# Kernel optimization log

Hardware: AMD Instinct MI355X
Metric: run time of the kernel (lower is better)

## Reference

```python
import jax, jax.numpy as jnp
import numpy as np

D_MODEL = 256
NHEAD = 8
NUM_EXPERTS = 5
LQ, LK, BATCH = 100, 1024, 16
LN_EPS = 1e-5


def setup_inputs() -> dict:
    key = jax.random.key(0)
    ks = jax.random.split(key, 12)
    d, E = D_MODEL, NUM_EXPERTS
    s = 1.0 / np.sqrt(d)
    return {
        "tgt": jax.random.normal(ks[0], (LQ, BATCH, d), jnp.float32),
        "memory": jax.random.normal(ks[1], (LK, BATCH, d), jnp.float32),
        "query_pos": jax.random.normal(ks[2], (LQ, BATCH, d), jnp.float32),
        "pos": jax.random.normal(ks[3], (LK, BATCH, d), jnp.float32),
        # per-expert MultiheadAttention params (packed q,k,v in_proj like torch)
        "w_in": jax.random.normal(ks[4], (E, 3 * d, d), jnp.float32) * s,
        "b_in": jnp.zeros((E, 3 * d), jnp.float32),
        "w_out": jax.random.normal(ks[5], (E, d, d), jnp.float32) * s,
        "b_out": jnp.zeros((E, d), jnp.float32),
        # gating network
        "w_gate": jax.random.normal(ks[6], (E, d), jnp.float32) * s,
        "b_gate": jnp.zeros((E,), jnp.float32),
        # LayerNorm
        "ln_gamma": jnp.ones((d,), jnp.float32),
        "ln_beta": jnp.zeros((d,), jnp.float32),
    }


def _moe_cross_attn(tgt, memory, query_pos, pos, w_in, b_in, w_out, b_out,
                    w_gate, b_gate, ln_gamma, ln_beta):
    Lq, B, d = tgt.shape
    H = NHEAD
    hd = d // H
    E = w_in.shape[0]
    Lk = memory.shape[0]

    # gating over (seq*batch, d) -> softmax over experts
    gate = jax.nn.softmax(tgt @ w_gate.T + b_gate, axis=-1)  # (Lq, B, E)

    q_emb = tgt + query_pos      # (Lq, B, d)
    k_emb = memory + pos         # (Lk, B, d)

    wq, wk, wv = w_in[:, :d], w_in[:, d:2 * d], w_in[:, 2 * d:]
    bq, bk, bv = b_in[:, :d], b_in[:, d:2 * d], b_in[:, 2 * d:]

    # batched projections across all experts (replaces python loop of MHA calls)
    q = jnp.einsum('lbd,eod->elbo', q_emb, wq) + bq[:, None, None, :]
    k = jnp.einsum('sbd,eod->esbo', k_emb, wk) + bk[:, None, None, :]
    v = jnp.einsum('sbd,eod->esbo', memory, wv) + bv[:, None, None, :]

    q = q.reshape(E, Lq, B, H, hd) * (1.0 / np.sqrt(hd))
    k = k.reshape(E, Lk, B, H, hd)
    v = v.reshape(E, Lk, B, H, hd)

    scores = jnp.einsum('elbhk,esbhk->ebhls', q, k)      # (E, B, H, Lq, Lk)
    attn = jax.nn.softmax(scores, axis=-1)
    ctx = jnp.einsum('ebhls,esbhk->elbhk', attn, v).reshape(E, Lq, B, d)

    out = jnp.einsum('elbd,eod->elbo', ctx, w_out) + b_out[:, None, None, :]

    # softmax-gated weighted combine of expert outputs
    mo = jnp.einsum('lbe,elbd->lbd', gate, out)

    x = tgt + mo  # dropout is identity (p=0.0)
    mu = jnp.mean(x, axis=-1, keepdims=True)
    var = jnp.var(x, axis=-1, keepdims=True)
    return (x - mu) * jax.lax.rsqrt(var + LN_EPS) * ln_gamma + ln_beta


def reference(tgt, memory, query_pos, pos, w_in, b_in, w_out, b_out,
              w_gate, b_gate, ln_gamma, ln_beta):
    return _moe_cross_attn(tgt, memory, query_pos, pos, w_in, b_in, w_out,
                           b_out, w_gate, b_gate, ln_gamma, ln_beta)
```

## Files before the change

### kernel.cpp

```cpp
#include <hip/hip_runtime.h>


typedef __bf16 bf16x8 __attribute__((ext_vector_type(8)));
typedef float f32x4 __attribute__((ext_vector_type(4)));
typedef unsigned int u32x4 __attribute__((ext_vector_type(4)));
typedef unsigned int u32x2 __attribute__((ext_vector_type(2)));
typedef unsigned short u16x4 __attribute__((ext_vector_type(4)));
typedef unsigned short us;

__device__ __forceinline__ us f2bf(float f) {
    unsigned u = __builtin_bit_cast(unsigned, f);
    u += 0x7FFFu + ((u >> 16) & 1u);
    return (us)(u >> 16);
}

__device__ __forceinline__ unsigned pack2(float lo, float hi) {
    return (unsigned)f2bf(lo) | ((unsigned)f2bf(hi) << 16);
}

__device__ __forceinline__ float bf2f(us v) {
    unsigned u = ((unsigned)v) << 16;
    return __builtin_bit_cast(float, u);
}

__device__ __forceinline__ bf16x8 ld_bf8(const us* p) {
    return __builtin_bit_cast(bf16x8, *reinterpret_cast<const u32x4*>(p));
}

__device__ __forceinline__ void gld_lds16(const us* g, us* l) {
    __builtin_amdgcn_global_load_lds(
        (const __attribute__((address_space(1))) unsigned int*)g,
        (__attribute__((address_space(3))) unsigned int*)l, 16, 0, 0);
}

__launch_bounds__(256)
__global__ void cvt_all(const float* __restrict__ tgt, const float* __restrict__ qpos,
                        const float* __restrict__ mem, const float* __restrict__ pos,
                        const float* __restrict__ w_in, const float* __restrict__ w_out,
                        const float* __restrict__ w_gate, const float* __restrict__ b_gate,
                        us* __restrict__ Aq, us* __restrict__ Ak, us* __restrict__ Av,
                        us* __restrict__ Wb, us* __restrict__ WOb,
                        float* __restrict__ Gate)
{
    const int bid = blockIdx.x;
    const int tid = threadIdx.x;
    if (bid < 400) {
        const int i = bid * 256 + tid;
        const int lane = tid & 63;
        const int row = i >> 6;
        f32x4 a = reinterpret_cast<const f32x4*>(tgt)[i];
        f32x4 b = reinterpret_cast<const f32x4*>(qpos)[i];
        u16x4 r;
#pragma unroll
        for (int j = 0; j < 4; ++j) r[j] = f2bf(a[j] + b[j]);
        reinterpret_cast<u16x4*>(Aq)[i] = r;
        float g[5];
#pragma unroll
        for (int e = 0; e < 5; ++e) {
            f32x4 wg = *reinterpret_cast<const f32x4*>(w_gate + e * 256 + 4 * lane);
            float p = a[0] * wg[0] + a[1] * wg[1] + a[2] * wg[2] + a[3] * wg[3];
#pragma unroll
            for (int off = 32; off >= 1; off >>= 1) p += __shfl_xor(p, off, 64);
            g[e] = p + b_gate[e];
        }
        float mx = g[0];
#pragma unroll
        for (int e = 1; e < 5; ++e) mx = fmaxf(mx, g[e]);
        float sm = 0.0f;
#pragma unroll
        for (int e = 0; e < 5; ++e) { g[e] = __expf(g[e] - mx); sm += g[e]; }
        const float invs = 1.0f / sm;
        if (lane == 0) {
#pragma unroll
            for (int e = 0; e < 5; ++e) Gate[row * 5 + e] = g[e] * invs;
        }
    } else if (bid < 4496) {
        int i = (bid - 400) * 256 + tid;
        f32x4 m = reinterpret_cast<const f32x4*>(mem)[i];
        f32x4 p = reinterpret_cast<const f32x4*>(pos)[i];
        u16x4 rk, rv;
#pragma unroll
        for (int j = 0; j < 4; ++j) { rk[j] = f2bf(m[j] + p[j]); rv[j] = f2bf(m[j]); }
        reinterpret_cast<u16x4*>(Ak)[i] = rk;
        reinterpret_cast<u16x4*>(Av)[i] = rv;
    } else if (bid < 5456) {
        int i = (bid - 4496) * 256 + tid;
        f32x4 a = reinterpret_cast<const f32x4*>(w_in)[i];
        u16x4 r;
#pragma unroll
        for (int j = 0; j < 4; ++j) r[j] = f2bf(a[j]);
        reinterpret_cast<u16x4*>(Wb)[i] = r;
    } else {
        int i = (bid - 5456) * 256 + tid;
        f32x4 a = reinterpret_cast<const f32x4*>(w_out)[i];
        u16x4 r;
#pragma unroll
        for (int j = 0; j < 4; ++j) r[j] = f2bf(a[j]);
        reinterpret_cast<u16x4*>(WOb)[i] = r;
    }
}

template <bool BF16OUT>
__device__ __forceinline__ void gemm_body(const us* __restrict__ A,
                                          const us* __restrict__ W,
                                          const float* __restrict__ bias,
                                          void* __restrict__ Cout,
                                          float scale, int M)
{
    const int row0 = blockIdx.x * 128;
    const int col0 = blockIdx.y * 128;
    __shared__ us As[2 * 8192];
    __shared__ us Bs[2 * 8192];
    const int tid  = threadIdx.x;
    const int lane = tid & 63;
    const int w    = tid >> 6;
    const int l15  = lane & 15;
    const int quad = lane >> 4;
    const int wm   = (w >> 1) * 64;
    const int wn   = (w & 1) * 64;
    const int srow = lane >> 3;
    const int gofs = ((lane & 7) ^ srow) * 8;

    auto stage = [&](int buf, int kt) {
#pragma unroll
        for (int cc = 0; cc < 4; ++cc) {
            const int c = w * 4 + cc;
            const int row = c * 8 + srow;
            gld_lds16(A + (size_t)(row0 + row) * 256 + kt * 64 + gofs,
                      &As[buf * 8192 + c * 512]);
            gld_lds16(W + (size_t)(col0 + row) * 256 + kt * 64 + gofs,
                      &Bs[buf * 8192 + c * 512]);
        }
    };

    f32x4 acc[4][4] = {};

    auto compute = [&](int cur) {
#pragma unroll
        for (int kh = 0; kh < 2; ++kh) {
            bf16x8 af[4], bf[4];
#pragma unroll
            for (int mi = 0; mi < 4; ++mi) {
                const int row = wm + mi * 16 + l15;
                const int seg = (kh * 4 + quad) ^ (row & 7);
                af[mi] = ld_bf8(&As[cur * 8192 + row * 64 + seg * 8]);
            }
#pragma unroll
            for (int ni = 0; ni < 4; ++ni) {
                const int col = wn + ni * 16 + l15;
                const int seg = (kh * 4 + quad) ^ (col & 7);
                bf[ni] = ld_bf8(&Bs[cur * 8192 + col * 64 + seg * 8]);
            }
#pragma unroll
            for (int mi = 0; mi < 4; ++mi)
#pragma unroll
                for (int ni = 0; ni < 4; ++ni)
                    acc[mi][ni] = __builtin_amdgcn_mfma_f32_16x16x32_bf16(bf[ni], af[mi], acc[mi][ni], 0, 0, 0);
        }
    };

    stage(0, 0);
    stage(1, 1);

#pragma unroll
    for (int kt = 0; kt < 4; ++kt) {
        const int cur = kt & 1;
        if (kt < 3) asm volatile("s_waitcnt vmcnt(8)" ::: "memory");
        else        asm volatile("s_waitcnt vmcnt(0)" ::: "memory");
        __builtin_amdgcn_s_barrier();
        __builtin_amdgcn_sched_barrier(0);
        compute(cur);
        if (kt < 2) {
            asm volatile("s_waitcnt lgkmcnt(0)" ::: "memory");
            __builtin_amdgcn_sched_barrier(0);
            __builtin_amdgcn_s_barrier();
            __builtin_amdgcn_sched_barrier(0);
            stage(cur, kt + 2);
        }
    }

#pragma unroll
    for (int mi = 0; mi < 4; ++mi) {
        const int row = row0 + wm + mi * 16 + l15;
        if (row < M) {
#pragma unroll
            for (int ni = 0; ni < 4; ++ni) {
                const int colb = col0 + wn + ni * 16 + quad * 4;
                const f32x4 b4 = *reinterpret_cast<const f32x4*>(bias + colb);
                if constexpr (BF16OUT) {
                    u32x2 pk;
                    pk[0] = pack2((acc[mi][ni][0] + b4[0]) * scale,
                                  (acc[mi][ni][1] + b4[1]) * scale);
                    pk[1] = pack2((acc[mi][ni][2] + b4[2]) * scale,
                                  (acc[mi][ni][3] + b4[3]) * scale);
                    *reinterpret_cast<u32x2*>(reinterpret_cast<us*>(Cout) + (size_t)row * 256 + colb) = pk;
                } else {
                    f32x4 v;
#pragma unroll
                    for (int r = 0; r < 4; ++r) v[r] = (acc[mi][ni][r] + b4[r]) * scale;
                    *reinterpret_cast<f32x4*>(reinterpret_cast<float*>(Cout) + (size_t)row * 256 + colb) = v;
                }
            }
        }
    }
}

__launch_bounds__(256)
__global__ void gemm_qkv(const us* __restrict__ Aq, const us* __restrict__ Ak,
                         const us* __restrict__ Av, const us* __restrict__ Wb,
                         const float* __restrict__ b_in,
                         us* __restrict__ Qb, us* __restrict__ Kb, us* __restrict__ Vb)
{
    const int z = blockIdx.z;
    if (z < 5) {
        if (blockIdx.x >= 13) return;
        gemm_body<true>(Aq, Wb + (size_t)z * 196608, b_in + (size_t)z * 768,
                        Qb + (size_t)z * 409600, 0.17677669529663687f, 1600);
    } else if (z < 10) {
        const int e = z - 5;
        gemm_body<true>(Ak, Wb + 65536 + (size_t)e * 196608, b_in + (size_t)e * 768 + 256,
                        Kb + (size_t)e * 4194304, 1.0f, 16384);
    } else {
        const int e = z - 10;
        gemm_body<true>(Av, Wb + 131072 + (size_t)e * 196608, b_in + (size_t)e * 768 + 512,
                        Vb + (size_t)e * 4194304, 1.0f, 16384);
    }
}

__launch_bounds__(256)
__global__ void gemm_og(const us* __restrict__ PO, const float* __restrict__ PL,
                        const us* __restrict__ WOb, const float* __restrict__ b_out,
                        float* __restrict__ OUTf)
{
    const int e = blockIdx.z;
    const us* W = WOb + (size_t)e * 65536;
    const float* bias = b_out + (size_t)e * 256;
    float* Cout = OUTf + (size_t)e * 409600;

    const int row0 = blockIdx.x * 128;
    const int col0 = blockIdx.y * 128;
    __shared__ us As[2 * 8192];
    __shared__ us Bs[2 * 8192];
    const int tid  = threadIdx.x;
    const int lane = tid & 63;
    const int w    = tid >> 6;
    const int l15  = lane & 15;
    const int quad = lane >> 4;
    const int wm   = (w >> 1) * 64;
    const int wn   = (w & 1) * 64;
    const int srow = lane >> 3;
    const int gofs = ((lane & 7) ^ srow) * 8;

    u32x4 POr[4][4];
    float Lr[4];

    auto loadA = [&](int kt) {
#pragma unroll
        for (int cc = 0; cc < 4; ++cc) {
            const int c = w * 4 + cc;
            int grow = row0 + c * 8 + srow;
            if (grow > 1599) grow = 1599;
            const int d0 = kt * 64 + gofs;
            const size_t base = (size_t)e * 409600 + (size_t)grow * 256 + d0;
#pragma unroll
            for (int s = 0; s < 4; ++s)
                POr[cc][s] = *reinterpret_cast<const u32x4*>(PO + base + (size_t)s * 2048000);
            const int l = grow >> 4, bb = grow & 15, h = d0 >> 5;
            float L = 0.0f;
#pragma unroll
            for (int s = 0; s < 4; ++s)
                L += PL[((((size_t)s * 5 + e) * 16 + bb) * 8 + h) * 128 + l];
            Lr[cc] = L;
        }
    };
    auto writeA = [&](int buf) {
#pragma unroll
        for (int cc = 0; cc < 4; ++cc) {
            const float inv = 1.0f / Lr[cc];
            u32x4 pk;
#pragma unroll
            for (int j = 0; j < 4; ++j) {
                float v0 = 0.0f, v1 = 0.0f;
#pragma unroll
                for (int s = 0; s < 4; ++s) {
                    const unsigned u = POr[cc][s][j];
                    v0 += __builtin_bit_cast(float, u << 16);
                    v1 += __builtin_bit_cast(float, u & 0xffff0000u);
                }
                pk[j] = pack2(v0 * inv, v1 * inv);
            }
            *reinterpret_cast<u32x4*>(&As[buf * 8192 + (w * 4 + cc) * 512 + lane * 8]) = pk;
        }
    };
    auto loadW = [&](int buf, int kt) {
#pragma unroll
        for (int cc = 0; cc < 4; ++cc) {
            const int c = w * 4 + cc;
            const int row = c * 8 + srow;
            gld_lds16(W + (size_t)(col0 + row) * 256 + kt * 64 + gofs,
                      &Bs[buf * 8192 + c * 512]);
        }
    };

    loadA(0);
    loadW(0, 0);
    writeA(0);
    __syncthreads();

    f32x4 acc[4][4] = {};

#pragma unroll
    for (int kt = 0; kt < 4; ++kt) {
        const int cur = kt & 1;
        if (kt < 3) {
            loadA(kt + 1);
            loadW(cur ^ 1, kt + 1);
        }
#pragma unroll
        for (int kh = 0; kh < 2; ++kh) {
            bf16x8 af[4], bf[4];
#pragma unroll
            for (int mi = 0; mi < 4; ++mi) {
                const int row = wm + mi * 16 + l15;
                const int seg = (kh * 4 + quad) ^ (row & 7);
                af[mi] = ld_bf8(&As[cur * 8192 + row * 64 + seg * 8]);
            }
#pragma unroll
            for (int ni = 0; ni < 4; ++ni) {
                const int col = wn + ni * 16 + l15;
                const int seg = (kh * 4 + quad) ^ (col & 7);
                bf[ni] = ld_bf8(&Bs[cur * 8192 + col * 64 + seg * 8]);
            }
#pragma unroll
            for (int mi = 0; mi < 4; ++mi)
#pragma unroll
                for (int ni = 0; ni < 4; ++ni)
                    acc[mi][ni] = __builtin_amdgcn_mfma_f32_16x16x32_bf16(bf[ni], af[mi], acc[mi][ni], 0, 0, 0);
        }
        if (kt < 3) {
            writeA(cur ^ 1);
            __syncthreads();
        }
    }

#pragma unroll
    for (int mi = 0; mi < 4; ++mi) {
        const int row = row0 + wm + mi * 16 + l15;
        if (row < 1600) {
#pragma unroll
            for (int ni = 0; ni < 4; ++ni) {
                const int colb = col0 + wn + ni * 16 + quad * 4;
                const f32x4 b4 = *reinterpret_cast<const f32x4*>(bias + colb);
                f32x4 v;
#pragma unroll
                for (int r = 0; r < 4; ++r) v[r] = acc[mi][ni][r] + b4[r];
                *reinterpret_cast<f32x4*>(Cout + (size_t)row * 256 + colb) = v;
            }
        }
    }
}

__device__ __forceinline__ int vrow(int d) { return d * 264 + 8 * (d >> 3); }

__launch_bounds__(512)
__global__ void attn(const us* __restrict__ Qb, const us* __restrict__ Kb,
                     const us* __restrict__ Vb, us* __restrict__ PO,
                     float* __restrict__ PL)
{
    const int h = blockIdx.x;
    const int z = blockIdx.y;
    const int s = blockIdx.z;
    const int e = z >> 4, b = z & 15;
    const int tid  = threadIdx.x;
    const int w    = tid >> 6;
    const int lane = tid & 63;
    const int l15  = lane & 15, quad = lane >> 4;
    __shared__ us Ks[256 * 32];
    __shared__ us Vs[8464];
    __shared__ us Ps[7][16 * 40];

    const int key0 = s * 256;
    {
        const int kl  = lane >> 2;
        const int seg = lane & 3;
        const us* kg = Kb + ((size_t)((e * 1024 + key0 + w * 16 + kl) * 16 + b)) * 256
                          + h * 32 + seg * 8;
        gld_lds16(kg, &Ks[w * 512]);
        gld_lds16(kg + (size_t)128 * 16 * 256, &Ks[4096 + w * 512]);

        const int kv = tid >> 2;
        const int sg = tid & 3;
        const us* vg = Vb + ((size_t)((e * 1024 + key0 + kv) * 16 + b)) * 256
                          + h * 32 + sg * 8;
        u32x4 v0 = *reinterpret_cast<const u32x4*>(vg);
        u32x4 v1 = *reinterpret_cast<const u32x4*>(vg + (size_t)128 * 16 * 256);
#pragma unroll
        for (int j = 0; j < 4; ++j) {
            const int d0 = sg * 8 + 2 * j;
            const int e0 = vrow(d0);
            const int e1 = e0 + 264;
            Vs[e0 + kv]       = (us)(v0[j] & 0xffff);
            Vs[e1 + kv]       = (us)(v0[j] >> 16);
            Vs[e0 + 128 + kv] = (us)(v1[j] & 0xffff);
            Vs[e1 + 128 + kv] = (us)(v1[j] >> 16);
        }
    }
    u32x4 qraw = {0u, 0u, 0u, 0u};
    if (w < 7) {
        const int l = w * 16 + l15;
        if (l < 100)
            qraw = *reinterpret_cast<const u32x4*>(
                Qb + ((size_t)((e * 100 + l) * 16 + b)) * 256 + h * 32 + quad * 8);
    }
    const bf16x8 qf = __builtin_bit_cast(bf16x8, qraw);

    __syncthreads();

    if (w >= 7) return;

    const f32x4 zacc = {};
    f32x4 o0 = {}, o1 = {};
    float lsum = 0.0f;

    for (int c = 0; c < 8; ++c) {
        bf16x8 kf0 = ld_bf8(&Ks[(c * 32 + l15) * 32 + quad * 8]);
        bf16x8 kf1 = ld_bf8(&Ks[(c * 32 + 16 + l15) * 32 + quad * 8]);
        f32x4 s0 = __builtin_amdgcn_mfma_f32_16x16x32_bf16(kf0, qf, zacc, 0, 0, 0);
        f32x4 s1 = __builtin_amdgcn_mfma_f32_16x16x32_bf16(kf1, qf, zacc, 0, 0, 0);
        float p0[4], p1[4];
#pragma unroll
        for (int r = 0; r < 4; ++r) {
            p0[r] = __expf(s0[r]);
            p1[r] = __expf(s1[r]);
            lsum += p0[r] + p1[r];
        }
        u32x2 w0, w1;
        w0[0] = pack2(p0[0], p0[1]);
        w0[1] = pack2(p0[2], p0[3]);
        w1[0] = pack2(p1[0], p1[1]);
        w1[1] = pack2(p1[2], p1[3]);
        *reinterpret_cast<u32x2*>(&Ps[w][l15 * 40 + quad * 4])      = w0;
        *reinterpret_cast<u32x2*>(&Ps[w][l15 * 40 + 16 + quad * 4]) = w1;
        bf16x8 pf  = ld_bf8(&Ps[w][l15 * 40 + quad * 8]);
        bf16x8 vf0 = ld_bf8(&Vs[vrow(l15) + c * 32 + quad * 8]);
        bf16x8 vf1 = ld_bf8(&Vs[vrow(16 + l15) + c * 32 + quad * 8]);
        o0 = __builtin_amdgcn_mfma_f32_16x16x32_bf16(pf, vf0, o0, 0, 0, 0);
        o1 = __builtin_amdgcn_mfma_f32_16x16x32_bf16(pf, vf1, o1, 0, 0, 0);
    }

    lsum += __shfl_xor(lsum, 16, 64);
    lsum += __shfl_xor(lsum, 32, 64);

#pragma unroll
    for (int r = 0; r < 4; ++r) {
        const int row = w * 16 + quad * 4 + r;
        if (row < 100) {
            const size_t o = (((size_t)((s * 5 + e) * 100 + row)) * 16 + b) * 256 + h * 32;
            PO[o + l15]      = f2bf(o0[r]);
            PO[o + 16 + l15] = f2bf(o1[r]);
        }
    }
    const int q = w * 16 + l15;
    if (quad == 0 && q < 100)
        PL[((((size_t)s * 5 + e) * 16 + b) * 8 + h) * 128 + q] = lsum;
}

__launch_bounds__(256)
__global__ void finalize(const float* __restrict__ tgt, const float* __restrict__ Gate,
                         const float* __restrict__ OUTf,
                         const float* __restrict__ gamma, const float* __restrict__ beta,
                         float* __restrict__ out)
{
    const int row = blockIdx.x;
    const int d = threadIdx.x;
    __shared__ float red[8];
    const float t = tgt[(size_t)row * 256 + d];

    float mo = 0.0f;
#pragma unroll
    for (int e = 0; e < 5; ++e)
        mo += Gate[row * 5 + e] * OUTf[((size_t)e * 1600 + row) * 256 + d];
    const float x = t + mo;

    float p1 = x, p2 = x * x;
#pragma unroll
    for (int off = 32; off >= 1; off >>= 1) {
        p1 += __shfl_xor(p1, off, 64);
        p2 += __shfl_xor(p2, off, 64);
    }
    if ((d & 63) == 0) { red[d >> 6] = p1; red[4 + (d >> 6)] = p2; }
    __syncthreads();
    const float mean = (red[0] + red[1] + red[2] + red[3]) * (1.0f / 256.0f);
    const float msq  = (red[4] + red[5] + red[6] + red[7]) * (1.0f / 256.0f);
    const float var  = msq - mean * mean;

    out[(size_t)row * 256 + d] = (x - mean) * rsqrtf(var + 1e-5f) * gamma[d] + beta[d];
}

extern "C" void kernel_launch(void* const* d_in, const int* in_sizes, int n_in,
                              void* d_out, int out_size, void* d_ws, size_t ws_size,
                              hipStream_t stream)
{
    const float* tgt    = (const float*)d_in[0];
    const float* mem    = (const float*)d_in[1];
    const float* qpos   = (const float*)d_in[2];
    const float* pos    = (const float*)d_in[3];
    const float* w_in   = (const float*)d_in[4];
    const float* b_in   = (const float*)d_in[5];
    const float* w_out  = (const float*)d_in[6];
    const float* b_out  = (const float*)d_in[7];
    const float* w_gate = (const float*)d_in[8];
    const float* b_gate = (const float*)d_in[9];
    const float* ln_g   = (const float*)d_in[10];
    const float* ln_b   = (const float*)d_in[11];
    float* out = (float*)d_out;

    char* p = (char*)d_ws;
    auto alloc = [&](size_t n) { char* r = p; p += (n + 255) & ~(size_t)255; return r; };

    us* Aq   = (us*)alloc(409600ull * 2);
    us* Ak   = (us*)alloc(4194304ull * 2);
    us* Av   = (us*)alloc(4194304ull * 2);
    us* Wb   = (us*)alloc(983040ull * 2);
    us* WOb  = (us*)alloc(327680ull * 2);
    us* Qb   = (us*)alloc(5ull * 409600 * 2);
    us* Kb   = (us*)alloc(5ull * 4194304 * 2);
    us* Vb   = (us*)alloc(5ull * 4194304 * 2);
    float* OUTf  = (float*)alloc(5ull * 409600 * 4);
    float* Gate  = (float*)alloc(1600ull * 5 * 4);
    us*    PO = (us*)d_ws;
    float* PL = (float*)((char*)d_ws + 16384000);

    cvt_all<<<5776, 256, 0, stream>>>(tgt, qpos, mem, pos, w_in, w_out,
                                      w_gate, b_gate, Aq, Ak, Av, Wb, WOb, Gate);

    gemm_qkv<<<dim3(128, 2, 15), 256, 0, stream>>>(Aq, Ak, Av, Wb, b_in, Qb, Kb, Vb);

    attn<<<dim3(8, 80, 4), 512, 0, stream>>>(Qb, Kb, Vb, PO, PL);

    gemm_og<<<dim3(13, 2, 5), 256, 0, stream>>>(PO, PL, WOb, b_out, OUTf);

    finalize<<<1600, 256, 0, stream>>>(tgt, Gate, OUTf, ln_g, ln_b, out);
}
```

Baseline: 207.7 us.

## Restructure QKV GEMM to keep A tile resident and loop over experts

The QKV projection kernel now loads a full 128x256 activation tile into LDS once per block and loops over all five experts, streaming weight fragments straight from global memory into registers with a three-buffer rotation. This replaces the previous 3D grid, in which each expert and column half re-staged the same activation rows through LDS, and aims to cut redundant activation traffic and launch a much smaller grid. In exchange, each block does five times more work with a larger accumulator set (8x4 tiles), which raises register pressure. The grid drops to 269 blocks, which may underfill the GPU's compute units and leaves the weight loads exposed to global memory latency.

```diff
diff --git a/kernel.cpp b/kernel.cpp
--- a/kernel.cpp
+++ b/kernel.cpp
@@ -100,130 +100,121 @@
     }
 }
 
-template <bool BF16OUT>
-__device__ __forceinline__ void gemm_body(const us* __restrict__ A,
-                                          const us* __restrict__ W,
-                                          const float* __restrict__ bias,
-                                          void* __restrict__ Cout,
-                                          float scale, int M)
-{
-    const int row0 = blockIdx.x * 128;
-    const int col0 = blockIdx.y * 128;
-    __shared__ us As[2 * 8192];
-    __shared__ us Bs[2 * 8192];
-    const int tid  = threadIdx.x;
-    const int lane = tid & 63;
-    const int w    = tid >> 6;
-    const int l15  = lane & 15;
-    const int quad = lane >> 4;
-    const int wm   = (w >> 1) * 64;
-    const int wn   = (w & 1) * 64;
-    const int srow = lane >> 3;
-    const int gofs = ((lane & 7) ^ srow) * 8;
-
-    auto stage = [&](int buf, int kt) {
-#pragma unroll
-        for (int cc = 0; cc < 4; ++cc) {
-            const int c = w * 4 + cc;
-            const int row = c * 8 + srow;
-            gld_lds16(A + (size_t)(row0 + row) * 256 + kt * 64 + gofs,
-                      &As[buf * 8192 + c * 512]);
-            gld_lds16(W + (size_t)(col0 + row) * 256 + kt * 64 + gofs,
-                      &Bs[buf * 8192 + c * 512]);
-        }
-    };
-
-    f32x4 acc[4][4] = {};
-
-    auto compute = [&](int cur) {
-#pragma unroll
-        for (int kh = 0; kh < 2; ++kh) {
-            bf16x8 af[4], bf[4];
-#pragma unroll
-            for (int mi = 0; mi < 4; ++mi) {
-                const int row = wm + mi * 16 + l15;
-                const int seg = (kh * 4 + quad) ^ (row & 7);
-                af[mi] = ld_bf8(&As[cur * 8192 + row * 64 + seg * 8]);
-            }
-#pragma unroll
-            for (int ni = 0; ni < 4; ++ni) {
-                const int col = wn + ni * 16 + l15;
-                const int seg = (kh * 4 + quad) ^ (col & 7);
-                bf[ni] = ld_bf8(&Bs[cur * 8192 + col * 64 + seg * 8]);
-            }
-#pragma unroll
-            for (int mi = 0; mi < 4; ++mi)
-#pragma unroll
-                for (int ni = 0; ni < 4; ++ni)
-                    acc[mi][ni] = __builtin_amdgcn_mfma_f32_16x16x32_bf16(bf[ni], af[mi], acc[mi][ni], 0, 0, 0);
-        }
-    };
-
-    stage(0, 0);
-    stage(1, 1);
-
-#pragma unroll
-    for (int kt = 0; kt < 4; ++kt) {
-        const int cur = kt & 1;
-        if (kt < 3) asm volatile("s_waitcnt vmcnt(8)" ::: "memory");
-        else        asm volatile("s_waitcnt vmcnt(0)" ::: "memory");
-        __builtin_amdgcn_s_barrier();
-        __builtin_amdgcn_sched_barrier(0);
-        compute(cur);
-        if (kt < 2) {
-            asm volatile("s_waitcnt lgkmcnt(0)" ::: "memory");
-            __builtin_amdgcn_sched_barrier(0);
-            __builtin_amdgcn_s_barrier();
-            __builtin_amdgcn_sched_barrier(0);
-            stage(cur, kt + 2);
-        }
-    }
-
-#pragma unroll
-    for (int mi = 0; mi < 4; ++mi) {
-        const int row = row0 + wm + mi * 16 + l15;
-        if (row < M) {
-#pragma unroll
-            for (int ni = 0; ni < 4; ++ni) {
-                const int colb = col0 + wn + ni * 16 + quad * 4;
-                const f32x4 b4 = *reinterpret_cast<const f32x4*>(bias + colb);
-                if constexpr (BF16OUT) {
-                    u32x2 pk;
-                    pk[0] = pack2((acc[mi][ni][0] + b4[0]) * scale,
-                                  (acc[mi][ni][1] + b4[1]) * scale);
-                    pk[1] = pack2((acc[mi][ni][2] + b4[2]) * scale,
-                                  (acc[mi][ni][3] + b4[3]) * scale);
-                    *reinterpret_cast<u32x2*>(reinterpret_cast<us*>(Cout) + (size_t)row * 256 + colb) = pk;
-                } else {
-                    f32x4 v;
-#pragma unroll
-                    for (int r = 0; r < 4; ++r) v[r] = (acc[mi][ni][r] + b4[r]) * scale;
-                    *reinterpret_cast<f32x4*>(reinterpret_cast<float*>(Cout) + (size_t)row * 256 + colb) = v;
-                }
-            }
-        }
-    }
-}
-
 __launch_bounds__(256)
 __global__ void gemm_qkv(const us* __restrict__ Aq, const us* __restrict__ Ak,
                          const us* __restrict__ Av, const us* __restrict__ Wb,
                          const float* __restrict__ b_in,
                          us* __restrict__ Qb, us* __restrict__ Kb, us* __restrict__ Vb)
 {
-    const int z = blockIdx.z;
-    if (z < 5) {
-        if (blockIdx.x >= 13) return;
-        gemm_body<true>(Aq, Wb + (size_t)z * 196608, b_in + (size_t)z * 768,
-                        Qb + (size_t)z * 409600, 0.17677669529663687f, 1600);
-    } else if (z < 10) {
-        const int e = z - 5;
-        gemm_body<true>(Ak, Wb + 65536 + (size_t)e * 196608, b_in + (size_t)e * 768 + 256,
-                        Kb + (size_t)e * 4194304, 1.0f, 16384);
+    const int bid = blockIdx.x;
+    const us* A;
+    const us* W0;
+    const float* bias0;
+    us* C0;
+    float scale;
+    int row0, M;
+    size_t cstride;
+    if (bid < 13) {
+        A = Aq; row0 = bid * 128; W0 = Wb; bias0 = b_in; C0 = Qb;
+        scale = 0.17677669529663687f; M = 1600; cstride = 409600;
+    } else if (bid < 141) {
+        A = Ak; row0 = (bid - 13) * 128; W0 = Wb + 65536; bias0 = b_in + 256; C0 = Kb;
+        scale = 1.0f; M = 16384; cstride = 4194304;
     } else {
-        const int e = z - 10;
-        gemm_body<true>(Av, Wb + 131072 + (size_t)e * 196608, b_in + (size_t)e * 768 + 512,
-                        Vb + (size_t)e * 4194304, 1.0f, 16384);
+        A = Av; row0 = (bid - 141) * 128; W0 = Wb + 131072; bias0 = b_in + 512; C0 = Vb;
+        scale = 1.0f; M = 16384; cstride = 4194304;
+    }
+
+    __shared__ us As[4 * 8192];
+    const int tid  = threadIdx.x;
+    const int lane = tid & 63;
+    const int w    = tid >> 6;
+    const int l15  = lane & 15;
+    const int quad = lane >> 4;
+    const int srow = lane >> 3;
+    const int gofs = ((lane & 7) ^ srow) * 8;
+    const int coln = w * 64;
+
+#pragma unroll
+    for (int cc = 0; cc < 16; ++cc)
+        gld_lds16(A + (size_t)(row0 + cc * 8 + srow) * 256 + w * 64 + gofs,
+                  &As[w * 8192 + cc * 512]);
+
+    f32x4 acc[8][4];
+    u32x4 bA[4], bB[4], bC[4];
+
+    auto loadB = [&](u32x4* dst, const us* W, int j) {
+#pragma unroll
+        for (int ni = 0; ni < 4; ++ni)
+            dst[ni] = *reinterpret_cast<const u32x4*>(
+                W + (size_t)(coln + ni * 16 + l15) * 256 + j * 32 + quad * 8);
+    };
+    auto kstep = [&](const u32x4* bq, int j) {
+        const int kts = j >> 1, kh = j & 1;
+#pragma unroll
+        for (int mi = 0; mi < 8; ++mi) {
+            const int row = mi * 16 + l15;
+            const int seg = (kh * 4 + quad) ^ (row & 7);
+            const bf16x8 af = ld_bf8(&As[kts * 8192 + row * 64 + seg * 8]);
+#pragma unroll
+            for (int ni = 0; ni < 4; ++ni)
+                acc[mi][ni] = __builtin_amdgcn_mfma_f32_16x16x32_bf16(
+                    __builtin_bit_cast(bf16x8, bq[ni]), af, acc[mi][ni], 0, 0, 0);
+        }
+    };
+
+    loadB(bA, W0, 0);
+    loadB(bB, W0, 1);
+    asm volatile("s_waitcnt vmcnt(8)" ::: "memory");
+    __builtin_amdgcn_s_barrier();
+    __builtin_amdgcn_sched_barrier(0);
+
+#pragma unroll 1
+    for (int e = 0; e < 5; ++e) {
+        const us* W = W0 + (size_t)e * 196608;
+        if (e) { loadB(bA, W, 0); loadB(bB, W, 1); }
+#pragma unroll
+        for (int mi = 0; mi < 8; ++mi)
+#pragma unroll
+            for (int ni = 0; ni < 4; ++ni) acc[mi][ni] = (f32x4){};
+
+        loadB(bC, W, 2);
+        kstep(bA, 0);
+        loadB(bA, W, 3);
+        kstep(bB, 1);
+        loadB(bB, W, 4);
+        kstep(bC, 2);
+        loadB(bC, W, 5);
+        kstep(bA, 3);
+        loadB(bA, W, 6);
+        kstep(bB, 4);
+        loadB(bB, W, 7);
+        kstep(bC, 5);
+        kstep(bA, 6);
+        kstep(bB, 7);
+
+        const float* bias = bias0 + (size_t)e * 768;
+        f32x4 b4[4];
+#pragma unroll
+        for (int ni = 0; ni < 4; ++ni)
+            b4[ni] = *reinterpret_cast<const f32x4*>(bias + coln + ni * 16 + quad * 4);
+        us* Ce = C0 + (size_t)e * cstride;
+#pragma unroll
+        for (int mi = 0; mi < 8; ++mi) {
+            const int row = row0 + mi * 16 + l15;
+            if (row < M) {
+#pragma unroll
+                for (int ni = 0; ni < 4; ++ni) {
+                    const int colb = coln + ni * 16 + quad * 4;
+                    u32x2 pk;
+                    pk[0] = pack2((acc[mi][ni][0] + b4[ni][0]) * scale,
+                                  (acc[mi][ni][1] + b4[ni][1]) * scale);
+                    pk[1] = pack2((acc[mi][ni][2] + b4[ni][2]) * scale,
+                                  (acc[mi][ni][3] + b4[ni][3]) * scale);
+                    *reinterpret_cast<u32x2*>(Ce + (size_t)row * 256 + colb) = pk;
+                }
+            }
+        }
     }
 }
 
@@ -534,7 +525,7 @@
     cvt_all<<<5776, 256, 0, stream>>>(tgt, qpos, mem, pos, w_in, w_out,
                                       w_gate, b_gate, Aq, Ak, Av, Wb, WOb, Gate);
 
-    gemm_qkv<<<dim3(128, 2, 15), 256, 0, stream>>>(Aq, Ak, Av, Wb, b_in, Qb, Kb, Vb);
+    gemm_qkv<<<269, 256, 0, stream>>>(Aq, Ak, Av, Wb, b_in, Qb, Kb, Vb);
 
     attn<<<dim3(8, 80, 4), 512, 0, stream>>>(Qb, Kb, Vb, PO, PL);
 
```

New measurement: 256.5 us. +23.5%, slower.

## Load QKV GEMM weights directly into registers and reorder grid for A-tile reuse

Applied to the files above, without the earlier changes.

The QKV projection GEMM stops staging the weight tile through shared memory; each lane loads its B fragments straight from global memory into registers. Only the A tile is double-buffered in LDS, which halves LDS use and lets the A load for the next k-step overlap compute. The grid is reordered so that the 15 projection jobs sharing a row block launch next to each other, which should improve L2 reuse of the activation tile. In exchange, weight fragments come from global or L2 without the swizzled coalescing of the staged path, and register pressure rises.

```diff
diff --git a/kernel.cpp b/kernel.cpp
--- a/kernel.cpp
+++ b/kernel.cpp
@@ -100,17 +100,33 @@
     }
 }
 
-template <bool BF16OUT>
-__device__ __forceinline__ void gemm_body(const us* __restrict__ A,
-                                          const us* __restrict__ W,
-                                          const float* __restrict__ bias,
-                                          void* __restrict__ Cout,
-                                          float scale, int M)
+__launch_bounds__(256)
+__global__ void gemm_qkv(const us* __restrict__ Aq, const us* __restrict__ Ak,
+                         const us* __restrict__ Av, const us* __restrict__ Wb,
+                         const float* __restrict__ b_in,
+                         us* __restrict__ Qb, us* __restrict__ Kb, us* __restrict__ Vb)
 {
-    const int row0 = blockIdx.x * 128;
+    const int zr  = blockIdx.x;
     const int col0 = blockIdx.y * 128;
+    const int rb  = blockIdx.z;
+    const us* A; const us* W; const float* bias; us* C;
+    float scale; int M;
+    if (zr < 5) {
+        if (rb >= 13) return;
+        A = Aq; W = Wb + (size_t)zr * 196608; bias = b_in + (size_t)zr * 768;
+        C = Qb + (size_t)zr * 409600; scale = 0.17677669529663687f; M = 1600;
+    } else if (zr < 10) {
+        const int e = zr - 5;
+        A = Ak; W = Wb + 65536 + (size_t)e * 196608; bias = b_in + (size_t)e * 768 + 256;
+        C = Kb + (size_t)e * 4194304; scale = 1.0f; M = 16384;
+    } else {
+        const int e = zr - 10;
+        A = Av; W = Wb + 131072 + (size_t)e * 196608; bias = b_in + (size_t)e * 768 + 512;
+        C = Vb + (size_t)e * 4194304; scale = 1.0f; M = 16384;
+    }
+    const int row0 = rb * 128;
+
     __shared__ us As[2 * 8192];
-    __shared__ us Bs[2 * 8192];
     const int tid  = threadIdx.x;
     const int lane = tid & 63;
     const int w    = tid >> 6;
@@ -121,24 +137,37 @@
     const int srow = lane >> 3;
     const int gofs = ((lane & 7) ^ srow) * 8;
 
-    auto stage = [&](int buf, int kt) {
+    auto stageA = [&](int buf, int kt) {
 #pragma unroll
         for (int cc = 0; cc < 4; ++cc) {
             const int c = w * 4 + cc;
-            const int row = c * 8 + srow;
-            gld_lds16(A + (size_t)(row0 + row) * 256 + kt * 64 + gofs,
+            gld_lds16(A + (size_t)(row0 + c * 8 + srow) * 256 + kt * 64 + gofs,
                       &As[buf * 8192 + c * 512]);
-            gld_lds16(W + (size_t)(col0 + row) * 256 + kt * 64 + gofs,
-                      &Bs[buf * 8192 + c * 512]);
         }
     };
 
     f32x4 acc[4][4] = {};
 
-    auto compute = [&](int cur) {
+    stageA(0, 0);
+
+#pragma unroll
+    for (int kt = 0; kt < 4; ++kt) {
+        const int cur = kt & 1;
+        u32x4 bf[2][4];
+#pragma unroll
+        for (int kh = 0; kh < 2; ++kh)
+#pragma unroll
+            for (int ni = 0; ni < 4; ++ni)
+                bf[kh][ni] = *reinterpret_cast<const u32x4*>(
+                    W + (size_t)(col0 + wn + ni * 16 + l15) * 256 + kt * 64 + kh * 32 + quad * 8);
+        if (kt < 3) stageA(cur ^ 1, kt + 1);
+        if (kt < 3) asm volatile("s_waitcnt vmcnt(4)" ::: "memory");
+        else        asm volatile("s_waitcnt vmcnt(0)" ::: "memory");
+        __builtin_amdgcn_s_barrier();
+        __builtin_amdgcn_sched_barrier(0);
 #pragma unroll
         for (int kh = 0; kh < 2; ++kh) {
-            bf16x8 af[4], bf[4];
+            bf16x8 af[4];
 #pragma unroll
             for (int mi = 0; mi < 4; ++mi) {
                 const int row = wm + mi * 16 + l15;
@@ -146,36 +175,17 @@
                 af[mi] = ld_bf8(&As[cur * 8192 + row * 64 + seg * 8]);
             }
 #pragma unroll
-            for (int ni = 0; ni < 4; ++ni) {
-                const int col = wn + ni * 16 + l15;
-                const int seg = (kh * 4 + quad) ^ (col & 7);
-                bf[ni] = ld_bf8(&Bs[cur * 8192 + col * 64 + seg * 8]);
-            }
-#pragma unroll
             for (int mi = 0; mi < 4; ++mi)
 #pragma unroll
                 for (int ni = 0; ni < 4; ++ni)
-                    acc[mi][ni] = __builtin_amdgcn_mfma_f32_16x16x32_bf16(bf[ni], af[mi], acc[mi][ni], 0, 0, 0);
-        }
-    };
-
-    stage(0, 0);
-    stage(1, 1);
-
-#pragma unroll
-    for (int kt = 0; kt < 4; ++kt) {
-        const int cur = kt & 1;
-        if (kt < 3) asm volatile("s_waitcnt vmcnt(8)" ::: "memory");
-        else        asm volatile("s_waitcnt vmcnt(0)" ::: "memory");
-        __builtin_amdgcn_s_barrier();
-        __builtin_amdgcn_sched_barrier(0);
-        compute(cur);
-        if (kt < 2) {
+                    acc[mi][ni] = __builtin_amdgcn_mfma_f32_16x16x32_bf16(
+                        __builtin_bit_cast(bf16x8, bf[kh][ni]), af[mi], acc[mi][ni], 0, 0, 0);
+        }
+        if (kt < 3) {
             asm volatile("s_waitcnt lgkmcnt(0)" ::: "memory");
             __builtin_amdgcn_sched_barrier(0);
             __builtin_amdgcn_s_barrier();
             __builtin_amdgcn_sched_barrier(0);
-            stage(cur, kt + 2);
         }
     }
 
@@ -187,43 +197,14 @@
             for (int ni = 0; ni < 4; ++ni) {
                 const int colb = col0 + wn + ni * 16 + quad * 4;
                 const f32x4 b4 = *reinterpret_cast<const f32x4*>(bias + colb);
-                if constexpr (BF16OUT) {
-                    u32x2 pk;
-                    pk[0] = pack2((acc[mi][ni][0] + b4[0]) * scale,
-                                  (acc[mi][ni][1] + b4[1]) * scale);
-                    pk[1] = pack2((acc[mi][ni][2] + b4[2]) * scale,
-                                  (acc[mi][ni][3] + b4[3]) * scale);
-                    *reinterpret_cast<u32x2*>(reinterpret_cast<us*>(Cout) + (size_t)row * 256 + colb) = pk;
-                } else {
-                    f32x4 v;
-#pragma unroll
-                    for (int r = 0; r < 4; ++r) v[r] = (acc[mi][ni][r] + b4[r]) * scale;
-                    *reinterpret_cast<f32x4*>(reinterpret_cast<float*>(Cout) + (size_t)row * 256 + colb) = v;
-                }
+                u32x2 pk;
+                pk[0] = pack2((acc[mi][ni][0] + b4[0]) * scale,
+                              (acc[mi][ni][1] + b4[1]) * scale);
+                pk[1] = pack2((acc[mi][ni][2] + b4[2]) * scale,
+                              (acc[mi][ni][3] + b4[3]) * scale);
+                *reinterpret_cast<u32x2*>(C + (size_t)row * 256 + colb) = pk;
             }
         }
-    }
-}
-
-__launch_bounds__(256)
-__global__ void gemm_qkv(const us* __restrict__ Aq, const us* __restrict__ Ak,
-                         const us* __restrict__ Av, const us* __restrict__ Wb,
-                         const float* __restrict__ b_in,
-                         us* __restrict__ Qb, us* __restrict__ Kb, us* __restrict__ Vb)
-{
-    const int z = blockIdx.z;
-    if (z < 5) {
-        if (blockIdx.x >= 13) return;
-        gemm_body<true>(Aq, Wb + (size_t)z * 196608, b_in + (size_t)z * 768,
-                        Qb + (size_t)z * 409600, 0.17677669529663687f, 1600);
-    } else if (z < 10) {
-        const int e = z - 5;
-        gemm_body<true>(Ak, Wb + 65536 + (size_t)e * 196608, b_in + (size_t)e * 768 + 256,
-                        Kb + (size_t)e * 4194304, 1.0f, 16384);
-    } else {
-        const int e = z - 10;
-        gemm_body<true>(Av, Wb + 131072 + (size_t)e * 196608, b_in + (size_t)e * 768 + 512,
-                        Vb + (size_t)e * 4194304, 1.0f, 16384);
     }
 }
 
@@ -534,7 +515,7 @@
     cvt_all<<<5776, 256, 0, stream>>>(tgt, qpos, mem, pos, w_in, w_out,
                                       w_gate, b_gate, Aq, Ak, Av, Wb, WOb, Gate);
 
-    gemm_qkv<<<dim3(128, 2, 15), 256, 0, stream>>>(Aq, Ak, Av, Wb, b_in, Qb, Kb, Vb);
+    gemm_qkv<<<dim3(15, 2, 128), 256, 0, stream>>>(Aq, Ak, Av, Wb, b_in, Qb, Kb, Vb);
 
     attn<<<dim3(8, 80, 4), 512, 0, stream>>>(Qb, Kb, Vb, PO, PL);
 
```

After: 224.5 us. 8.1% more time.
